# Optimization experiments

Hardware: AMD Instinct MI355X
Metric: run time of the kernel (lower is better)

## Reference

```python
import jax, jax.numpy as jnp
import numpy as np

N_VOCAB_TOTAL = 32064  # n_vocab + n_nts
D_MODEL = 256


def setup_inputs() -> dict:
    key = jax.random.key(0)
    ks = jax.random.split(key, 8)
    d = D_MODEL
    tokens = jax.random.randint(ks[0], (64, 4095), 0, N_VOCAB_TOTAL, dtype=jnp.int32)
    # embedding_tgt: normal with std 1/sqrt(d) (reset_parameters)
    E = jax.random.normal(ks[1], (N_VOCAB_TOTAL, d), dtype=jnp.float32) / jnp.sqrt(jnp.float32(d))
    s_in = 1.0 / np.sqrt(3 * d)
    s_h = 1.0 / np.sqrt(d)
    W_in = jax.random.uniform(ks[2], (d, 3 * d), jnp.float32, -s_in, s_in)  # Linear(3d, d)
    b_in = jax.random.uniform(ks[3], (d,), jnp.float32, -s_in, s_in)
    W1 = jax.random.uniform(ks[4], (d, d), jnp.float32, -s_h, s_h)
    b1 = jax.random.uniform(ks[5], (d,), jnp.float32, -s_h, s_h)
    W2 = jax.random.uniform(ks[6], (d, d), jnp.float32, -s_h, s_h)
    b2 = jax.random.uniform(ks[7], (d,), jnp.float32, -s_h, s_h)
    return {"tokens": tokens, "E": E, "W_in": W_in, "b_in": b_in,
            "W1": W1, "b1": b1, "W2": W2, "b2": b2}


def _bin_agg(roots, left, right, W_in, b_in, W1, b1, W2, b2):
    # skipmlp_binary_agg: root + hidden(inp(cat([root,left,right])))
    # hidden = ELU -> Linear -> ELU -> Linear  (nlayers=2)
    x = jnp.concatenate([roots, left, right], axis=-1)        # [..., 3d]
    h = x @ W_in.T + b_in                                     # inp: Linear(3d, d)
    h = jax.nn.elu(h) @ W1.T + b1
    h = jax.nn.elu(h) @ W2.T + b2
    return roots + h


def reference(tokens, E, W_in, b_in, W1, b1, W2, b2):
    # tokens: [B, N] heap-ordered perfect binary trees, N = 2^(D+1)-1.
    B, N = tokens.shape
    n_leaves = (N + 1) // 2
    emb = E[tokens]                                           # [B, N, d] gather
    cur = emb[:, N - n_leaves:]                               # leaf level, [B, 2^D, d]
    level = n_leaves // 2
    while level >= 1:                                          # fixed D iterations
        roots = emb[:, level - 1: 2 * level - 1]               # [B, level, d]
        left = cur[:, 0::2]
        right = cur[:, 1::2]
        cur = _bin_agg(roots, left, right, W_in, b_in, W1, b1, W2, b2)
        level //= 2
    return cur[:, 0]                                           # [B, d] root embeddings
```

## Files before the change

kernel.cpp:

```cpp
#include <hip/hip_runtime.h>
#include <stdint.h>


typedef __attribute__((ext_vector_type(8))) short short8;
typedef __attribute__((ext_vector_type(4))) float f32x4;

typedef const __attribute__((address_space(1))) unsigned int* gas_ptr;
typedef __attribute__((address_space(3))) unsigned int* las_ptr;

#define TOK_N 4095

__device__ __forceinline__ unsigned short f32_to_bf16(float f) {
    union { float f; unsigned u; } v; v.f = f;
    return (unsigned short)((v.u + 0x7fffu + ((v.u >> 16) & 1u)) >> 16);
}
__device__ __forceinline__ float bf16_to_f32(unsigned short u) {
    union { unsigned u; float f; } v; v.u = ((unsigned)u) << 16; return v.f;
}

__global__ void convert_f32_bf16(const float* __restrict__ E,
                                 const float* __restrict__ Win,
                                 const float* __restrict__ W1,
                                 const float* __restrict__ W2,
                                 unsigned short* __restrict__ Ebf,
                                 unsigned short* __restrict__ Winbf,
                                 unsigned short* __restrict__ W1bf,
                                 unsigned short* __restrict__ W2bf) {
    const int nE = 32064 * 256, nWin = 256 * 768, nW = 256 * 256;
    const int total4 = (nE + nWin + 2 * nW) >> 2;
    for (int i = blockIdx.x * blockDim.x + threadIdx.x; i < total4;
         i += gridDim.x * blockDim.x) {
        int idx = i << 2;
        const float* src; unsigned short* dst; int off;
        if (idx < nE)                  { src = E;   dst = Ebf;   off = idx; }
        else if (idx < nE + nWin)      { src = Win; dst = Winbf; off = idx - nE; }
        else if (idx < nE + nWin + nW) { src = W1;  dst = W1bf;  off = idx - nE - nWin; }
        else                           { src = W2;  dst = W2bf;  off = idx - nE - nWin - nW; }
        float4 f = *(const float4*)(src + off);
        ushort4 o;
        o.x = f32_to_bf16(f.x); o.y = f32_to_bf16(f.y);
        o.z = f32_to_bf16(f.z); o.w = f32_to_bf16(f.w);
        *(ushort4*)(dst + off) = o;
    }
}

template<int MT, int WROW, typename F>
__device__ __forceinline__ void run_pass(const unsigned short* __restrict__ Xs,
                                         const unsigned short* __restrict__ wlane,
                                         int kbase, f32x4 (&acc)[MT][4],
                                         int l15, int q, F&& late)
{
    const int xm = l15 & 7;
    short8 bb[2][4], bt[2][4];
#pragma unroll
    for (int d = 0; d < 2; ++d)
#pragma unroll
        for (int nt = 0; nt < 4; ++nt)
            bb[d][nt] = *(const short8*)(wlane + (size_t)(nt * 16) * WROW + kbase + d * 32);
#pragma unroll
    for (int d = 0; d < 2; ++d)
#pragma unroll
        for (int nt = 0; nt < 4; ++nt)
            bt[d][nt] = *(const short8*)(wlane + (size_t)(nt * 16) * WROW + kbase + (6 + d) * 32);
#pragma unroll
    for (int k = 0; k < 8; ++k) {
        if (k == 4) {
            __builtin_amdgcn_sched_barrier(0);
            late();
            __builtin_amdgcn_sched_barrier(0);
        }
        short8 a[MT];
        const int sl = (((4 * k + q) ^ xm) << 3);
#pragma unroll
        for (int mt = 0; mt < MT; ++mt)
            a[mt] = *(const short8*)(Xs + (mt * 16 + l15) * 256 + sl);
#pragma unroll
        for (int mt = 0; mt < MT; ++mt)
#pragma unroll
            for (int nt = 0; nt < 4; ++nt)
                acc[mt][nt] = __builtin_amdgcn_mfma_f32_16x16x32_bf16(
                    a[mt], (k >= 6) ? bt[k - 6][nt] : bb[k & 1][nt],
                    acc[mt][nt], 0, 0, 0);
        if (k < 4) {
#pragma unroll
            for (int nt = 0; nt < 4; ++nt)
                bb[k & 1][nt] = *(const short8*)(wlane + (size_t)(nt * 16) * WROW + kbase + (k + 2) * 32);
        }
    }
}

template<int MT, int LAST>
__global__ __launch_bounds__(256, 3)
void tree_level(const int* __restrict__ tokens,
                const unsigned short* __restrict__ Ebf,
                const unsigned short* __restrict__ Win,
                const unsigned short* __restrict__ W1,
                const unsigned short* __restrict__ W2,
                const float* __restrict__ b_in,
                const float* __restrict__ b1,
                const float* __restrict__ b2,
                const unsigned short* __restrict__ cur_in,
                unsigned short* __restrict__ cur_out,
                float* __restrict__ final_out,
                int L, int logL, int first)
{
    constexpr int R = MT * 16;
    __shared__ unsigned short Xs[R * 256];
    __shared__ unsigned short Hs[R * 256];
    __shared__ unsigned short Gs[R * 256];

    const int tid  = threadIdx.x;
    const int lane = tid & 63;
    const int wid  = tid >> 6;
    const int l15  = lane & 15;
    const int q    = lane >> 4;
    const int n0   = wid * 64;
    const int blk  = blockIdx.x;

    auto gather = [&](int p, unsigned short* dst) {
#pragma unroll
        for (int t = 0; t < R / 8; ++t) {
            const int base_r = wid * (R / 4) + t * 2;
            const int r = base_r + (lane >> 5);
            const unsigned short* src;
            {
                int g = blk * R + r;
                int b = g >> logL;
                int i = g - (b << logL);
                if (p == 0) {
                    int tok = tokens[b * TOK_N + (L - 1) + i];
                    src = Ebf + (size_t)tok * 256;
                } else if (first) {
                    int tok = tokens[b * TOK_N + 2047 + 2 * i + (p - 1)];
                    src = Ebf + (size_t)tok * 256;
                } else {
                    src = cur_in + ((size_t)b * (2 * L) + 2 * i + (p - 1)) * 256;
                }
            }
            const int c = (lane & 31) ^ (r & 7);
            __builtin_amdgcn_global_load_lds(
                (gas_ptr)(const void*)(src + c * 8),
                (las_ptr)(void*)(dst + base_r * 256), 16, 0, 0);
        }
    };

    float bva[4], bvb[4], bvc[4];
#pragma unroll
    for (int nt = 0; nt < 4; ++nt) {
        bva[nt] = b_in[n0 + nt * 16 + l15];
        bvb[nt] = b1[n0 + nt * 16 + l15];
        bvc[nt] = b2[n0 + nt * 16 + l15];
    }

    f32x4 acc[MT][4];
    auto init_acc = [&](const float* bv) {
#pragma unroll
        for (int mt = 0; mt < MT; ++mt)
#pragma unroll
            for (int nt = 0; nt < 4; ++nt)
                acc[mt][nt] = (f32x4){bv[nt], bv[nt], bv[nt], bv[nt]};
    };
    auto store_elu = [&](unsigned short* dst) {
#pragma unroll
        for (int mt = 0; mt < MT; ++mt)
#pragma unroll
            for (int nt = 0; nt < 4; ++nt)
#pragma unroll
                for (int rr = 0; rr < 4; ++rr) {
                    int row = mt * 16 + q * 4 + rr;
                    int col = n0 + nt * 16 + l15;
                    float h = acc[mt][nt][rr];
                    h = h > 0.f ? h : (__expf(h) - 1.f);
                    int slot = (col >> 3) ^ (row & 7);
                    dst[row * 256 + slot * 8 + (col & 7)] = f32_to_bf16(h);
                }
    };

    gather(0, Xs);
    __syncthreads();
    init_acc(bva);
    const unsigned short* winlane = Win + q * 8 + (size_t)(n0 + l15) * 768;
    run_pass<MT, 768>(Xs, winlane, 0, acc, l15, q, [&]() {
        gather(1, Hs);
        gather(2, Gs);
    });
    __syncthreads();
    run_pass<MT, 768>(Hs, winlane, 256, acc, l15, q, []() {});
    __syncthreads();
    run_pass<MT, 768>(Gs, winlane, 512, acc, l15, q, []() {});
    store_elu(Hs);
    __syncthreads();

    init_acc(bvb);
    run_pass<MT, 256>(Hs, W1 + q * 8 + (size_t)(n0 + l15) * 256, 0, acc, l15, q, []() {});
    __syncthreads();
    store_elu(Hs);
    __syncthreads();

    init_acc(bvc);
    run_pass<MT, 256>(Hs, W2 + q * 8 + (size_t)(n0 + l15) * 256, 0, acc, l15, q, []() {});

    if (LAST) {
#pragma unroll
        for (int mt = 0; mt < MT; ++mt)
#pragma unroll
            for (int nt = 0; nt < 4; ++nt)
#pragma unroll
                for (int rr = 0; rr < 4; ++rr) {
                    int row = mt * 16 + q * 4 + rr;
                    int col = n0 + nt * 16 + l15;
                    int slot = (col >> 3) ^ (row & 7);
                    float o = acc[mt][nt][rr] +
                              bf16_to_f32(Xs[row * 256 + slot * 8 + (col & 7)]);
                    final_out[(size_t)(blk * R + row) * 256 + col] = o;
                }
    } else {
        __syncthreads();
#pragma unroll
        for (int mt = 0; mt < MT; ++mt)
#pragma unroll
            for (int nt = 0; nt < 4; ++nt)
#pragma unroll
                for (int rr = 0; rr < 4; ++rr) {
                    int row = mt * 16 + q * 4 + rr;
                    int col = n0 + nt * 16 + l15;
                    int slot = (col >> 3) ^ (row & 7);
                    float o = acc[mt][nt][rr] +
                              bf16_to_f32(Xs[row * 256 + slot * 8 + (col & 7)]);
                    Gs[row * 256 + slot * 8 + (col & 7)] = f32_to_bf16(o);
                }
        __syncthreads();
        const int s   = tid & 31;
        const int sub = tid >> 5;
#pragma unroll
        for (int it = 0; it < R / 8; ++it) {
            int r = it * 8 + sub;
            int c = s ^ (r & 7);
            *(short8*)(cur_out + (size_t)(blk * R + r) * 256 + c * 8) =
                *(const short8*)(Gs + r * 256 + s * 8);
        }
    }
}

template<int MT, int LAST>
static void launch_level(const int* tokens, const unsigned short* Ebf,
                         const unsigned short* Win, const unsigned short* W1,
                         const unsigned short* W2, const float* b_in,
                         const float* b1, const float* b2,
                         const unsigned short* cin, unsigned short* cout,
                         float* out, int L, int first, hipStream_t stream) {
    int logL = 31 - __builtin_clz((unsigned)L);
    int blocks = (64 * L) / (16 * MT);
    tree_level<MT, LAST><<<dim3(blocks), dim3(256), 0, stream>>>(
        tokens, Ebf, Win, W1, W2, b_in, b1, b2, cin, cout, out, L, logL, first);
}

extern "C" void kernel_launch(void* const* d_in, const int* in_sizes, int n_in,
                              void* d_out, int out_size, void* d_ws, size_t ws_size,
                              hipStream_t stream) {
    const int*   tokens = (const int*)  d_in[0];
    const float* E      = (const float*)d_in[1];
    const float* W_in   = (const float*)d_in[2];
    const float* b_in   = (const float*)d_in[3];
    const float* W1     = (const float*)d_in[4];
    const float* b1     = (const float*)d_in[5];
    const float* W2     = (const float*)d_in[6];
    const float* b2     = (const float*)d_in[7];
    float* out = (float*)d_out;
    char* ws = (char*)d_ws;

    unsigned short* Ebf   = (unsigned short*)(ws);
    unsigned short* Winbf = (unsigned short*)(ws + 16416768);
    unsigned short* W1bf  = (unsigned short*)(ws + 16809984);
    unsigned short* W2bf  = (unsigned short*)(ws + 16941056);
    unsigned short* curA  = (unsigned short*)(ws + 17072128);
    unsigned short* curB  = (unsigned short*)(ws + 50626560);

    convert_f32_bf16<<<1024, 256, 0, stream>>>(E, W_in, W1, W2,
                                               Ebf, Winbf, W1bf, W2bf);

    const unsigned short* cin = curB;
    unsigned short* cout = curA;
    int first = 1;
    for (int L = 1024; L >= 1; L >>= 1) {
        int last = (L == 1);
        if (L >= 256)
            launch_level<2, 0>(tokens, Ebf, Winbf, W1bf, W2bf, b_in, b1, b2,
                               cin, cout, nullptr, L, first, stream);
        else if (!last)
            launch_level<1, 0>(tokens, Ebf, Winbf, W1bf, W2bf, b_in, b1, b2,
                               cin, cout, nullptr, L, first, stream);
        else
            launch_level<1, 1>(tokens, Ebf, Winbf, W1bf, W2bf, b_in, b1, b2,
                               cin, cout, out, L, first, stream);
        cin = cout;
        cout = (cout == curA) ? curB : curA;
        first = 0;
    }
}
```

Measured before the change: 567.0 us.

## Fuse conversion and all tree levels into one persistent cooperative kernel

Replaces the conversion kernel and the eleven per-level launches with a single cooperative persistent kernel that converts weights and embeddings to bf16, then loops over tree levels with grid-wide syncs between them. Blocks stride over 32-row tiles using a rotating three-buffer LDS scheme and prefetch the next tile's root gather during the W1 pass. This removes launch gaps and tail underutilisation on small levels, at the cost of grid.sync overhead and fixed 32-row tiles for the tiny late levels, which leave most blocks idle.

```diff
diff --git a/kernel.cpp b/kernel.cpp
--- a/kernel.cpp
+++ b/kernel.cpp
@@ -1,5 +1,8 @@
 #include <hip/hip_runtime.h>
+#include <hip/hip_cooperative_groups.h>
 #include <stdint.h>
+
+namespace cg = cooperative_groups;
 
 
 typedef __attribute__((ext_vector_type(8))) short short8;
@@ -9,6 +12,7 @@
 typedef __attribute__((address_space(3))) unsigned int* las_ptr;
 
 #define TOK_N 4095
+#define RR 32
 
 __device__ __forceinline__ unsigned short f32_to_bf16(float f) {
     union { float f; unsigned u; } v; v.f = f;
@@ -18,36 +22,10 @@
     union { unsigned u; float f; } v; v.u = ((unsigned)u) << 16; return v.f;
 }
 
-__global__ void convert_f32_bf16(const float* __restrict__ E,
-                                 const float* __restrict__ Win,
-                                 const float* __restrict__ W1,
-                                 const float* __restrict__ W2,
-                                 unsigned short* __restrict__ Ebf,
-                                 unsigned short* __restrict__ Winbf,
-                                 unsigned short* __restrict__ W1bf,
-                                 unsigned short* __restrict__ W2bf) {
-    const int nE = 32064 * 256, nWin = 256 * 768, nW = 256 * 256;
-    const int total4 = (nE + nWin + 2 * nW) >> 2;
-    for (int i = blockIdx.x * blockDim.x + threadIdx.x; i < total4;
-         i += gridDim.x * blockDim.x) {
-        int idx = i << 2;
-        const float* src; unsigned short* dst; int off;
-        if (idx < nE)                  { src = E;   dst = Ebf;   off = idx; }
-        else if (idx < nE + nWin)      { src = Win; dst = Winbf; off = idx - nE; }
-        else if (idx < nE + nWin + nW) { src = W1;  dst = W1bf;  off = idx - nE - nWin; }
-        else                           { src = W2;  dst = W2bf;  off = idx - nE - nWin - nW; }
-        float4 f = *(const float4*)(src + off);
-        ushort4 o;
-        o.x = f32_to_bf16(f.x); o.y = f32_to_bf16(f.y);
-        o.z = f32_to_bf16(f.z); o.w = f32_to_bf16(f.w);
-        *(ushort4*)(dst + off) = o;
-    }
-}
-
-template<int MT, int WROW, typename F>
+template<int WROW, typename F>
 __device__ __forceinline__ void run_pass(const unsigned short* __restrict__ Xs,
                                          const unsigned short* __restrict__ wlane,
-                                         int kbase, f32x4 (&acc)[MT][4],
+                                         int kbase, f32x4 (&acc)[2][4],
                                          int l15, int q, F&& late)
 {
     const int xm = l15 & 7;
@@ -69,13 +47,13 @@
             late();
             __builtin_amdgcn_sched_barrier(0);
         }
-        short8 a[MT];
+        short8 a[2];
         const int sl = (((4 * k + q) ^ xm) << 3);
 #pragma unroll
-        for (int mt = 0; mt < MT; ++mt)
+        for (int mt = 0; mt < 2; ++mt)
             a[mt] = *(const short8*)(Xs + (mt * 16 + l15) * 256 + sl);
 #pragma unroll
-        for (int mt = 0; mt < MT; ++mt)
+        for (int mt = 0; mt < 2; ++mt)
 #pragma unroll
             for (int nt = 0; nt < 4; ++nt)
                 acc[mt][nt] = __builtin_amdgcn_mfma_f32_16x16x32_bf16(
@@ -89,25 +67,46 @@
     }
 }
 
-template<int MT, int LAST>
 __global__ __launch_bounds__(256, 3)
-void tree_level(const int* __restrict__ tokens,
-                const unsigned short* __restrict__ Ebf,
-                const unsigned short* __restrict__ Win,
-                const unsigned short* __restrict__ W1,
-                const unsigned short* __restrict__ W2,
-                const float* __restrict__ b_in,
-                const float* __restrict__ b1,
-                const float* __restrict__ b2,
-                const unsigned short* __restrict__ cur_in,
-                unsigned short* __restrict__ cur_out,
-                float* __restrict__ final_out,
-                int L, int logL, int first)
+void tree_all(const int* __restrict__ tokens,
+              const float* __restrict__ Ef,
+              const float* __restrict__ Winf,
+              const float* __restrict__ b_in,
+              const float* __restrict__ W1f,
+              const float* __restrict__ b1,
+              const float* __restrict__ W2f,
+              const float* __restrict__ b2,
+              unsigned short* __restrict__ Ebf,
+              unsigned short* __restrict__ Win,
+              unsigned short* __restrict__ W1,
+              unsigned short* __restrict__ W2,
+              unsigned short* __restrict__ curA,
+              unsigned short* __restrict__ curB,
+              float* __restrict__ out)
 {
-    constexpr int R = MT * 16;
-    __shared__ unsigned short Xs[R * 256];
-    __shared__ unsigned short Hs[R * 256];
-    __shared__ unsigned short Gs[R * 256];
+    __shared__ unsigned short S[3][RR * 256];
+    cg::grid_group grid = cg::this_grid();
+
+    {
+        const int nE = 32064 * 256, nWin = 256 * 768, nW = 256 * 256;
+        const int total4 = (nE + nWin + 2 * nW) >> 2;
+        for (int i = blockIdx.x * blockDim.x + threadIdx.x; i < total4;
+             i += gridDim.x * blockDim.x) {
+            int idx = i << 2;
+            const float* src; unsigned short* dst; int off;
+            if (idx < nE)                  { src = Ef;  dst = Ebf; off = idx; }
+            else if (idx < nE + nWin)      { src = Winf; dst = Win; off = idx - nE; }
+            else if (idx < nE + nWin + nW) { src = W1f; dst = W1;  off = idx - nE - nWin; }
+            else                           { src = W2f; dst = W2;  off = idx - nE - nWin - nW; }
+            float4 f = *(const float4*)(src + off);
+            ushort4 o;
+            o.x = f32_to_bf16(f.x); o.y = f32_to_bf16(f.y);
+            o.z = f32_to_bf16(f.z); o.w = f32_to_bf16(f.w);
+            *(ushort4*)(dst + off) = o;
+        }
+    }
+    __threadfence();
+    grid.sync();
 
     const int tid  = threadIdx.x;
     const int lane = tid & 63;
@@ -115,34 +114,6 @@
     const int l15  = lane & 15;
     const int q    = lane >> 4;
     const int n0   = wid * 64;
-    const int blk  = blockIdx.x;
-
-    auto gather = [&](int p, unsigned short* dst) {
-#pragma unroll
-        for (int t = 0; t < R / 8; ++t) {
-            const int base_r = wid * (R / 4) + t * 2;
-            const int r = base_r + (lane >> 5);
-            const unsigned short* src;
-            {
-                int g = blk * R + r;
-                int b = g >> logL;
-                int i = g - (b << logL);
-                if (p == 0) {
-                    int tok = tokens[b * TOK_N + (L - 1) + i];
-                    src = Ebf + (size_t)tok * 256;
-                } else if (first) {
-                    int tok = tokens[b * TOK_N + 2047 + 2 * i + (p - 1)];
-                    src = Ebf + (size_t)tok * 256;
-                } else {
-                    src = cur_in + ((size_t)b * (2 * L) + 2 * i + (p - 1)) * 256;
-                }
-            }
-            const int c = (lane & 31) ^ (r & 7);
-            __builtin_amdgcn_global_load_lds(
-                (gas_ptr)(const void*)(src + c * 8),
-                (las_ptr)(void*)(dst + base_r * 256), 16, 0, 0);
-        }
-    };
 
     float bva[4], bvb[4], bvc[4];
 #pragma unroll
@@ -151,18 +122,21 @@
         bvb[nt] = b1[n0 + nt * 16 + l15];
         bvc[nt] = b2[n0 + nt * 16 + l15];
     }
-
-    f32x4 acc[MT][4];
+    const unsigned short* winlane = Win + q * 8 + (size_t)(n0 + l15) * 768;
+    const unsigned short* w1lane  = W1  + q * 8 + (size_t)(n0 + l15) * 256;
+    const unsigned short* w2lane  = W2  + q * 8 + (size_t)(n0 + l15) * 256;
+
+    f32x4 acc[2][4];
     auto init_acc = [&](const float* bv) {
 #pragma unroll
-        for (int mt = 0; mt < MT; ++mt)
+        for (int mt = 0; mt < 2; ++mt)
 #pragma unroll
             for (int nt = 0; nt < 4; ++nt)
                 acc[mt][nt] = (f32x4){bv[nt], bv[nt], bv[nt], bv[nt]};
     };
     auto store_elu = [&](unsigned short* dst) {
 #pragma unroll
-        for (int mt = 0; mt < MT; ++mt)
+        for (int mt = 0; mt < 2; ++mt)
 #pragma unroll
             for (int nt = 0; nt < 4; ++nt)
 #pragma unroll
@@ -176,83 +150,118 @@
                 }
     };
 
-    gather(0, Xs);
-    __syncthreads();
-    init_acc(bva);
-    const unsigned short* winlane = Win + q * 8 + (size_t)(n0 + l15) * 768;
-    run_pass<MT, 768>(Xs, winlane, 0, acc, l15, q, [&]() {
-        gather(1, Hs);
-        gather(2, Gs);
-    });
-    __syncthreads();
-    run_pass<MT, 768>(Hs, winlane, 256, acc, l15, q, []() {});
-    __syncthreads();
-    run_pass<MT, 768>(Gs, winlane, 512, acc, l15, q, []() {});
-    store_elu(Hs);
-    __syncthreads();
-
-    init_acc(bvb);
-    run_pass<MT, 256>(Hs, W1 + q * 8 + (size_t)(n0 + l15) * 256, 0, acc, l15, q, []() {});
-    __syncthreads();
-    store_elu(Hs);
-    __syncthreads();
-
-    init_acc(bvc);
-    run_pass<MT, 256>(Hs, W2 + q * 8 + (size_t)(n0 + l15) * 256, 0, acc, l15, q, []() {});
-
-    if (LAST) {
-#pragma unroll
-        for (int mt = 0; mt < MT; ++mt)
-#pragma unroll
-            for (int nt = 0; nt < 4; ++nt)
-#pragma unroll
-                for (int rr = 0; rr < 4; ++rr) {
-                    int row = mt * 16 + q * 4 + rr;
-                    int col = n0 + nt * 16 + l15;
-                    int slot = (col >> 3) ^ (row & 7);
-                    float o = acc[mt][nt][rr] +
-                              bf16_to_f32(Xs[row * 256 + slot * 8 + (col & 7)]);
-                    final_out[(size_t)(blk * R + row) * 256 + col] = o;
+    int r = 0, l = 1, m = 2;
+    const unsigned short* cin = curB;
+    unsigned short* cout = curA;
+
+    for (int L = 1024; L >= 1; L >>= 1) {
+        const int logL  = 31 - __builtin_clz((unsigned)L);
+        const int tiles = 2 * L;
+        const int first = (L == 1024);
+        const int last  = (L == 1);
+
+        auto gather = [&](int p, int tile, unsigned short* dst) {
+#pragma unroll
+            for (int it = 0; it < RR / 8; ++it) {
+                const int base_r = wid * (RR / 4) + it * 2;
+                const int rw = base_r + (lane >> 5);
+                const unsigned short* src;
+                {
+                    int g = tile * RR + rw;
+                    int b = g >> logL;
+                    int i = g - (b << logL);
+                    if (p == 0) {
+                        int tok = tokens[b * TOK_N + (L - 1) + i];
+                        src = Ebf + (size_t)tok * 256;
+                    } else if (first) {
+                        int tok = tokens[b * TOK_N + 2047 + 2 * i + (p - 1)];
+                        src = Ebf + (size_t)tok * 256;
+                    } else {
+                        src = cin + ((size_t)b * (2 * L) + 2 * i + (p - 1)) * 256;
+                    }
                 }
-    } else {
-        __syncthreads();
-#pragma unroll
-        for (int mt = 0; mt < MT; ++mt)
-#pragma unroll
-            for (int nt = 0; nt < 4; ++nt)
-#pragma unroll
-                for (int rr = 0; rr < 4; ++rr) {
-                    int row = mt * 16 + q * 4 + rr;
-                    int col = n0 + nt * 16 + l15;
-                    int slot = (col >> 3) ^ (row & 7);
-                    float o = acc[mt][nt][rr] +
-                              bf16_to_f32(Xs[row * 256 + slot * 8 + (col & 7)]);
-                    Gs[row * 256 + slot * 8 + (col & 7)] = f32_to_bf16(o);
+                const int c = (lane & 31) ^ (rw & 7);
+                __builtin_amdgcn_global_load_lds(
+                    (gas_ptr)(const void*)(src + c * 8),
+                    (las_ptr)(void*)(dst + base_r * 256), 16, 0, 0);
+            }
+        };
+
+        int t = blockIdx.x;
+        if (t < tiles) gather(0, t, S[r]);
+        for (; t < tiles; t += gridDim.x) {
+            __syncthreads();
+
+            init_acc(bva);
+            run_pass<768>(S[r], winlane, 0, acc, l15, q, [&]() {
+                gather(1, t, S[l]);
+                gather(2, t, S[m]);
+            });
+            __syncthreads();
+            run_pass<768>(S[l], winlane, 256, acc, l15, q, []() {});
+            __syncthreads();
+            run_pass<768>(S[m], winlane, 512, acc, l15, q, []() {});
+            store_elu(S[l]);
+            __syncthreads();
+
+            init_acc(bvb);
+            const bool pre = (t + (int)gridDim.x) < tiles;
+            run_pass<256>(S[l], w1lane, 0, acc, l15, q, [&]() {
+                if (pre) gather(0, t + gridDim.x, S[m]);
+            });
+            __syncthreads();
+            store_elu(S[l]);
+            __syncthreads();
+
+            init_acc(bvc);
+            run_pass<256>(S[l], w2lane, 0, acc, l15, q, []() {});
+
+            if (last) {
+#pragma unroll
+                for (int mt = 0; mt < 2; ++mt)
+#pragma unroll
+                    for (int nt = 0; nt < 4; ++nt)
+#pragma unroll
+                        for (int rr = 0; rr < 4; ++rr) {
+                            int row = mt * 16 + q * 4 + rr;
+                            int col = n0 + nt * 16 + l15;
+                            int slot = (col >> 3) ^ (row & 7);
+                            float o = acc[mt][nt][rr] +
+                                      bf16_to_f32(S[r][row * 256 + slot * 8 + (col & 7)]);
+                            out[(size_t)(t * RR + row) * 256 + col] = o;
+                        }
+            } else {
+#pragma unroll
+                for (int mt = 0; mt < 2; ++mt)
+#pragma unroll
+                    for (int nt = 0; nt < 4; ++nt)
+#pragma unroll
+                        for (int rr = 0; rr < 4; ++rr) {
+                            int row = mt * 16 + q * 4 + rr;
+                            int col = n0 + nt * 16 + l15;
+                            int slot = (col >> 3) ^ (row & 7);
+                            int a = row * 256 + slot * 8 + (col & 7);
+                            float o = acc[mt][nt][rr] + bf16_to_f32(S[r][a]);
+                            S[r][a] = f32_to_bf16(o);
+                        }
+                __syncthreads();
+                const int s   = tid & 31;
+                const int sub = tid >> 5;
+#pragma unroll
+                for (int it = 0; it < RR / 8; ++it) {
+                    int rw = it * 8 + sub;
+                    int c = s ^ (rw & 7);
+                    *(short8*)(cout + (size_t)(t * RR + rw) * 256 + c * 8) =
+                        *(const short8*)(S[r] + rw * 256 + s * 8);
                 }
-        __syncthreads();
-        const int s   = tid & 31;
-        const int sub = tid >> 5;
-#pragma unroll
-        for (int it = 0; it < R / 8; ++it) {
-            int r = it * 8 + sub;
-            int c = s ^ (r & 7);
-            *(short8*)(cur_out + (size_t)(blk * R + r) * 256 + c * 8) =
-                *(const short8*)(Gs + r * 256 + s * 8);
+            }
+            int nr = m; m = l; l = r; r = nr;
         }
+        __threadfence();
+        grid.sync();
+        cin = cout;
+        cout = (cout == curA) ? curB : curA;
     }
-}
-
-template<int MT, int LAST>
-static void launch_level(const int* tokens, const unsigned short* Ebf,
-                         const unsigned short* Win, const unsigned short* W1,
-                         const unsigned short* W2, const float* b_in,
-                         const float* b1, const float* b2,
-                         const unsigned short* cin, unsigned short* cout,
-                         float* out, int L, int first, hipStream_t stream) {
-    int logL = 31 - __builtin_clz((unsigned)L);
-    int blocks = (64 * L) / (16 * MT);
-    tree_level<MT, LAST><<<dim3(blocks), dim3(256), 0, stream>>>(
-        tokens, Ebf, Win, W1, W2, b_in, b1, b2, cin, cout, out, L, logL, first);
 }
 
 extern "C" void kernel_launch(void* const* d_in, const int* in_sizes, int n_in,
@@ -276,25 +285,16 @@
     unsigned short* curA  = (unsigned short*)(ws + 17072128);
     unsigned short* curB  = (unsigned short*)(ws + 50626560);
 
-    convert_f32_bf16<<<1024, 256, 0, stream>>>(E, W_in, W1, W2,
-                                               Ebf, Winbf, W1bf, W2bf);
-
-    const unsigned short* cin = curB;
-    unsigned short* cout = curA;
-    int first = 1;
-    for (int L = 1024; L >= 1; L >>= 1) {
-        int last = (L == 1);
-        if (L >= 256)
-            launch_level<2, 0>(tokens, Ebf, Winbf, W1bf, W2bf, b_in, b1, b2,
-                               cin, cout, nullptr, L, first, stream);
-        else if (!last)
-            launch_level<1, 0>(tokens, Ebf, Winbf, W1bf, W2bf, b_in, b1, b2,
-                               cin, cout, nullptr, L, first, stream);
-        else
-            launch_level<1, 1>(tokens, Ebf, Winbf, W1bf, W2bf, b_in, b1, b2,
-                               cin, cout, out, L, first, stream);
-        cin = cout;
-        cout = (cout == curA) ? curB : curA;
-        first = 0;
-    }
-}
+    int maxB = 0;
+    hipOccupancyMaxActiveBlocksPerMultiprocessor(&maxB, (const void*)tree_all, 256, 0);
+    if (maxB < 1) maxB = 1;
+    if (maxB > 3) maxB = 3;
+    int grid = 256 * maxB;
+
+    void* args[] = { (void*)&tokens, (void*)&E, (void*)&W_in, (void*)&b_in,
+                     (void*)&W1, (void*)&b1, (void*)&W2, (void*)&b2,
+                     (void*)&Ebf, (void*)&Winbf, (void*)&W1bf, (void*)&W2bf,
+                     (void*)&curA, (void*)&curB, (void*)&out };
+    hipLaunchCooperativeKernel((const void*)tree_all, dim3(grid), dim3(256),
+                               args, 0, stream);
+}
```

Result: slower. 1.905 ms (+235.9%).

## Fuse small tree levels into one per-batch tail kernel and prefetch weights across passes

Applied to the files above, without the earlier changes.

Levels 32 and below now run in a single tree_tail kernel, one block per batch element. Intermediate results stay in shared memory across levels, which removes six kernel launches and their global round trips. The weight-fragment pipeline is rewritten as a 4-deep register ring that preloads the next matrix's first K-slices during the current pass, so the next GEMM does not stall on weight loads. All tree_level launches are fixed at 32 rows per block. The tail kernel has only 64 blocks and computes padded rows for small levels, so it runs at low occupancy and does wasted work.

```diff
diff --git a/kernel.cpp b/kernel.cpp
--- a/kernel.cpp
+++ b/kernel.cpp
@@ -9,6 +9,7 @@
 typedef __attribute__((address_space(3))) unsigned int* las_ptr;
 
 #define TOK_N 4095
+#define RR 32
 
 __device__ __forceinline__ unsigned short f32_to_bf16(float f) {
     union { float f; unsigned u; } v; v.f = f;
@@ -44,24 +45,16 @@
     }
 }
 
-template<int MT, int WROW, typename F>
+template<typename F>
 __device__ __forceinline__ void run_pass(const unsigned short* __restrict__ Xs,
-                                         const unsigned short* __restrict__ wlane,
-                                         int kbase, f32x4 (&acc)[MT][4],
+                                         const unsigned short* __restrict__ curW,
+                                         int curNT, int curK,
+                                         const unsigned short* __restrict__ nxtW,
+                                         int nxtNT, int nxtK, bool hasNext,
+                                         short8 (&bb)[4][4], f32x4 (&acc)[2][4],
                                          int l15, int q, F&& late)
 {
     const int xm = l15 & 7;
-    short8 bb[2][4], bt[2][4];
-#pragma unroll
-    for (int d = 0; d < 2; ++d)
-#pragma unroll
-        for (int nt = 0; nt < 4; ++nt)
-            bb[d][nt] = *(const short8*)(wlane + (size_t)(nt * 16) * WROW + kbase + d * 32);
-#pragma unroll
-    for (int d = 0; d < 2; ++d)
-#pragma unroll
-        for (int nt = 0; nt < 4; ++nt)
-            bt[d][nt] = *(const short8*)(wlane + (size_t)(nt * 16) * WROW + kbase + (6 + d) * 32);
 #pragma unroll
     for (int k = 0; k < 8; ++k) {
         if (k == 4) {
@@ -69,27 +62,31 @@
             late();
             __builtin_amdgcn_sched_barrier(0);
         }
-        short8 a[MT];
+        short8 a0, a1;
         const int sl = (((4 * k + q) ^ xm) << 3);
-#pragma unroll
-        for (int mt = 0; mt < MT; ++mt)
-            a[mt] = *(const short8*)(Xs + (mt * 16 + l15) * 256 + sl);
-#pragma unroll
-        for (int mt = 0; mt < MT; ++mt)
-#pragma unroll
-            for (int nt = 0; nt < 4; ++nt)
-                acc[mt][nt] = __builtin_amdgcn_mfma_f32_16x16x32_bf16(
-                    a[mt], (k >= 6) ? bt[k - 6][nt] : bb[k & 1][nt],
-                    acc[mt][nt], 0, 0, 0);
+        a0 = *(const short8*)(Xs + l15 * 256 + sl);
+        a1 = *(const short8*)(Xs + (16 + l15) * 256 + sl);
+        short8 bc[4];
+#pragma unroll
+        for (int nt = 0; nt < 4; ++nt) bc[nt] = bb[k & 3][nt];
+#pragma unroll
+        for (int nt = 0; nt < 4; ++nt)
+            acc[0][nt] = __builtin_amdgcn_mfma_f32_16x16x32_bf16(a0, bc[nt], acc[0][nt], 0, 0, 0);
+#pragma unroll
+        for (int nt = 0; nt < 4; ++nt)
+            acc[1][nt] = __builtin_amdgcn_mfma_f32_16x16x32_bf16(a1, bc[nt], acc[1][nt], 0, 0, 0);
         if (k < 4) {
 #pragma unroll
             for (int nt = 0; nt < 4; ++nt)
-                bb[k & 1][nt] = *(const short8*)(wlane + (size_t)(nt * 16) * WROW + kbase + (k + 2) * 32);
-        }
-    }
-}
-
-template<int MT, int LAST>
+                bb[k & 3][nt] = *(const short8*)(curW + nt * curNT + curK + (k + 4) * 32);
+        } else if (hasNext) {
+#pragma unroll
+            for (int nt = 0; nt < 4; ++nt)
+                bb[k & 3][nt] = *(const short8*)(nxtW + nt * nxtNT + nxtK + (k - 4) * 32);
+        }
+    }
+}
+
 __global__ __launch_bounds__(256, 3)
 void tree_level(const int* __restrict__ tokens,
                 const unsigned short* __restrict__ Ebf,
@@ -101,13 +98,11 @@
                 const float* __restrict__ b2,
                 const unsigned short* __restrict__ cur_in,
                 unsigned short* __restrict__ cur_out,
-                float* __restrict__ final_out,
                 int L, int logL, int first)
 {
-    constexpr int R = MT * 16;
-    __shared__ unsigned short Xs[R * 256];
-    __shared__ unsigned short Hs[R * 256];
-    __shared__ unsigned short Gs[R * 256];
+    __shared__ unsigned short S0[RR * 256];
+    __shared__ unsigned short S1[RR * 256];
+    __shared__ unsigned short S2[RR * 256];
 
     const int tid  = threadIdx.x;
     const int lane = tid & 63;
@@ -116,15 +111,17 @@
     const int q    = lane >> 4;
     const int n0   = wid * 64;
     const int blk  = blockIdx.x;
+    const int s    = tid & 31;
+    const int sub  = tid >> 5;
 
     auto gather = [&](int p, unsigned short* dst) {
 #pragma unroll
-        for (int t = 0; t < R / 8; ++t) {
-            const int base_r = wid * (R / 4) + t * 2;
+        for (int it = 0; it < 4; ++it) {
+            const int base_r = wid * 8 + it * 2;
             const int r = base_r + (lane >> 5);
             const unsigned short* src;
             {
-                int g = blk * R + r;
+                int g = blk * RR + r;
                 int b = g >> logL;
                 int i = g - (b << logL);
                 if (p == 0) {
@@ -151,18 +148,21 @@
         bvb[nt] = b1[n0 + nt * 16 + l15];
         bvc[nt] = b2[n0 + nt * 16 + l15];
     }
-
-    f32x4 acc[MT][4];
+    const unsigned short* winlane = Win + q * 8 + (size_t)(n0 + l15) * 768;
+    const unsigned short* w1lane  = W1  + q * 8 + (size_t)(n0 + l15) * 256;
+    const unsigned short* w2lane  = W2  + q * 8 + (size_t)(n0 + l15) * 256;
+
+    f32x4 acc[2][4];
     auto init_acc = [&](const float* bv) {
 #pragma unroll
-        for (int mt = 0; mt < MT; ++mt)
+        for (int mt = 0; mt < 2; ++mt)
 #pragma unroll
             for (int nt = 0; nt < 4; ++nt)
                 acc[mt][nt] = (f32x4){bv[nt], bv[nt], bv[nt], bv[nt]};
     };
     auto store_elu = [&](unsigned short* dst) {
 #pragma unroll
-        for (int mt = 0; mt < MT; ++mt)
+        for (int mt = 0; mt < 2; ++mt)
 #pragma unroll
             for (int nt = 0; nt < 4; ++nt)
 #pragma unroll
@@ -176,83 +176,232 @@
                 }
     };
 
-    gather(0, Xs);
-    __syncthreads();
+    short8 bb[4][4];
+    auto noop = []() {};
+
+    gather(0, S0);
+#pragma unroll
+    for (int j = 0; j < 4; ++j)
+#pragma unroll
+        for (int nt = 0; nt < 4; ++nt)
+            bb[j][nt] = *(const short8*)(winlane + nt * 12288 + j * 32);
+    __syncthreads();
+
     init_acc(bva);
+    run_pass(S0, winlane, 12288, 0, winlane, 12288, 256, true, bb, acc, l15, q,
+             [&]() { gather(1, S1); gather(2, S2); });
+    __syncthreads();
+    run_pass(S1, winlane, 12288, 256, winlane, 12288, 512, true, bb, acc, l15, q, noop);
+    run_pass(S2, winlane, 12288, 512, w1lane, 4096, 0, true, bb, acc, l15, q, noop);
+    __syncthreads();
+    store_elu(S1);
+    __syncthreads();
+
+    init_acc(bvb);
+    run_pass(S1, w1lane, 4096, 0, w2lane, 4096, 0, true, bb, acc, l15, q, noop);
+    __syncthreads();
+    store_elu(S1);
+    __syncthreads();
+
+    init_acc(bvc);
+    run_pass(S1, w2lane, 4096, 0, (const unsigned short*)nullptr, 0, 0, false,
+             bb, acc, l15, q, noop);
+
+#pragma unroll
+    for (int mt = 0; mt < 2; ++mt)
+#pragma unroll
+        for (int nt = 0; nt < 4; ++nt)
+#pragma unroll
+            for (int rr = 0; rr < 4; ++rr) {
+                int row = mt * 16 + q * 4 + rr;
+                int col = n0 + nt * 16 + l15;
+                int slot = (col >> 3) ^ (row & 7);
+                float o = acc[mt][nt][rr] +
+                          bf16_to_f32(S0[row * 256 + slot * 8 + (col & 7)]);
+                S1[row * 256 + slot * 8 + (col & 7)] = f32_to_bf16(o);
+            }
+    __syncthreads();
+#pragma unroll
+    for (int it = 0; it < 4; ++it) {
+        int r = it * 8 + sub;
+        int c = s ^ (r & 7);
+        *(short8*)(cur_out + (size_t)(blk * RR + r) * 256 + c * 8) =
+            *(const short8*)(S1 + r * 256 + s * 8);
+    }
+}
+
+__global__ __launch_bounds__(256, 2)
+void tree_tail(const int* __restrict__ tokens,
+               const unsigned short* __restrict__ Ebf,
+               const unsigned short* __restrict__ Win,
+               const unsigned short* __restrict__ W1,
+               const unsigned short* __restrict__ W2,
+               const float* __restrict__ b_in,
+               const float* __restrict__ b1,
+               const float* __restrict__ b2,
+               const unsigned short* __restrict__ cur_in,
+               float* __restrict__ out)
+{
+    __shared__ unsigned short S0[RR * 256];
+    __shared__ unsigned short S1[RR * 256];
+    __shared__ unsigned short S2[RR * 256];
+    __shared__ unsigned short P[RR * 256];
+
+    const int b    = blockIdx.x;
+    const int tid  = threadIdx.x;
+    const int lane = tid & 63;
+    const int wid  = tid >> 6;
+    const int l15  = lane & 15;
+    const int q    = lane >> 4;
+    const int n0   = wid * 64;
+    const int s    = tid & 31;
+    const int sub  = tid >> 5;
+
+    float bva[4], bvb[4], bvc[4];
+#pragma unroll
+    for (int nt = 0; nt < 4; ++nt) {
+        bva[nt] = b_in[n0 + nt * 16 + l15];
+        bvb[nt] = b1[n0 + nt * 16 + l15];
+        bvc[nt] = b2[n0 + nt * 16 + l15];
+    }
     const unsigned short* winlane = Win + q * 8 + (size_t)(n0 + l15) * 768;
-    run_pass<MT, 768>(Xs, winlane, 0, acc, l15, q, [&]() {
-        gather(1, Hs);
-        gather(2, Gs);
-    });
-    __syncthreads();
-    run_pass<MT, 768>(Hs, winlane, 256, acc, l15, q, []() {});
-    __syncthreads();
-    run_pass<MT, 768>(Gs, winlane, 512, acc, l15, q, []() {});
-    store_elu(Hs);
-    __syncthreads();
-
-    init_acc(bvb);
-    run_pass<MT, 256>(Hs, W1 + q * 8 + (size_t)(n0 + l15) * 256, 0, acc, l15, q, []() {});
-    __syncthreads();
-    store_elu(Hs);
-    __syncthreads();
-
-    init_acc(bvc);
-    run_pass<MT, 256>(Hs, W2 + q * 8 + (size_t)(n0 + l15) * 256, 0, acc, l15, q, []() {});
-
-    if (LAST) {
-#pragma unroll
-        for (int mt = 0; mt < MT; ++mt)
+    const unsigned short* w1lane  = W1  + q * 8 + (size_t)(n0 + l15) * 256;
+    const unsigned short* w2lane  = W2  + q * 8 + (size_t)(n0 + l15) * 256;
+
+    f32x4 acc[2][4];
+    auto init_acc = [&](const float* bv) {
+#pragma unroll
+        for (int mt = 0; mt < 2; ++mt)
+#pragma unroll
+            for (int nt = 0; nt < 4; ++nt)
+                acc[mt][nt] = (f32x4){bv[nt], bv[nt], bv[nt], bv[nt]};
+    };
+    auto store_elu = [&](unsigned short* dst) {
+#pragma unroll
+        for (int mt = 0; mt < 2; ++mt)
 #pragma unroll
             for (int nt = 0; nt < 4; ++nt)
 #pragma unroll
                 for (int rr = 0; rr < 4; ++rr) {
                     int row = mt * 16 + q * 4 + rr;
                     int col = n0 + nt * 16 + l15;
+                    float h = acc[mt][nt][rr];
+                    h = h > 0.f ? h : (__expf(h) - 1.f);
                     int slot = (col >> 3) ^ (row & 7);
-                    float o = acc[mt][nt][rr] +
-                              bf16_to_f32(Xs[row * 256 + slot * 8 + (col & 7)]);
-                    final_out[(size_t)(blk * R + row) * 256 + col] = o;
+                    dst[row * 256 + slot * 8 + (col & 7)] = f32_to_bf16(h);
                 }
-    } else {
+    };
+
+    short8 bb[4][4];
+    auto noop = []() {};
+
+    auto groot = [&](int L) {
+#pragma unroll
+        for (int it = 0; it < 4; ++it) {
+            const int base_r = wid * 8 + it * 2;
+            const int r = base_r + (lane >> 5);
+            const int i = (r < L) ? r : 0;
+            int tok = tokens[b * TOK_N + (L - 1) + i];
+            const unsigned short* src = Ebf + (size_t)tok * 256;
+            const int c = (lane & 31) ^ (r & 7);
+            __builtin_amdgcn_global_load_lds(
+                (gas_ptr)(const void*)(src + c * 8),
+                (las_ptr)(void*)(S0 + base_r * 256), 16, 0, 0);
+        }
+    };
+    auto gchild_g = [&](int p, unsigned short* dst) {
+#pragma unroll
+        for (int it = 0; it < 4; ++it) {
+            const int base_r = wid * 8 + it * 2;
+            const int r = base_r + (lane >> 5);
+            const unsigned short* src = cur_in + ((size_t)b * 64 + 2 * r + (p - 1)) * 256;
+            const int c = (lane & 31) ^ (r & 7);
+            __builtin_amdgcn_global_load_lds(
+                (gas_ptr)(const void*)(src + c * 8),
+                (las_ptr)(void*)(dst + base_r * 256), 16, 0, 0);
+        }
+    };
+    auto gchild_p = [&](int L) {
+#pragma unroll
+        for (int it = 0; it < 4; ++it) {
+            int r = it * 8 + sub;
+            int i = (r < L) ? r : 0;
+            int c = s ^ (r & 7);
+            int sl = 2 * i, sr = 2 * i + 1;
+            *(short8*)(S1 + r * 256 + s * 8) = *(const short8*)(P + sl * 256 + ((c ^ (sl & 7))) * 8);
+            *(short8*)(S2 + r * 256 + s * 8) = *(const short8*)(P + sr * 256 + ((c ^ (sr & 7))) * 8);
+        }
+    };
+
+#pragma unroll
+    for (int j = 0; j < 4; ++j)
+#pragma unroll
+        for (int nt = 0; nt < 4; ++nt)
+            bb[j][nt] = *(const short8*)(winlane + nt * 12288 + j * 32);
+
+    for (int L = 32; L >= 1; L >>= 1) {
+        const bool lastJob = (L == 1);
+        groot(L);
+        if (L == 32) { gchild_g(1, S1); gchild_g(2, S2); }
+        else         gchild_p(L);
         __syncthreads();
-#pragma unroll
-        for (int mt = 0; mt < MT; ++mt)
-#pragma unroll
-            for (int nt = 0; nt < 4; ++nt)
-#pragma unroll
-                for (int rr = 0; rr < 4; ++rr) {
-                    int row = mt * 16 + q * 4 + rr;
-                    int col = n0 + nt * 16 + l15;
-                    int slot = (col >> 3) ^ (row & 7);
-                    float o = acc[mt][nt][rr] +
-                              bf16_to_f32(Xs[row * 256 + slot * 8 + (col & 7)]);
-                    Gs[row * 256 + slot * 8 + (col & 7)] = f32_to_bf16(o);
-                }
+
+        init_acc(bva);
+        run_pass(S0, winlane, 12288, 0, winlane, 12288, 256, true, bb, acc, l15, q, noop);
+        run_pass(S1, winlane, 12288, 256, winlane, 12288, 512, true, bb, acc, l15, q, noop);
+        run_pass(S2, winlane, 12288, 512, w1lane, 4096, 0, true, bb, acc, l15, q, noop);
         __syncthreads();
-        const int s   = tid & 31;
-        const int sub = tid >> 5;
-#pragma unroll
-        for (int it = 0; it < R / 8; ++it) {
-            int r = it * 8 + sub;
-            int c = s ^ (r & 7);
-            *(short8*)(cur_out + (size_t)(blk * R + r) * 256 + c * 8) =
-                *(const short8*)(Gs + r * 256 + s * 8);
-        }
-    }
-}
-
-template<int MT, int LAST>
-static void launch_level(const int* tokens, const unsigned short* Ebf,
-                         const unsigned short* Win, const unsigned short* W1,
-                         const unsigned short* W2, const float* b_in,
-                         const float* b1, const float* b2,
-                         const unsigned short* cin, unsigned short* cout,
-                         float* out, int L, int first, hipStream_t stream) {
-    int logL = 31 - __builtin_clz((unsigned)L);
-    int blocks = (64 * L) / (16 * MT);
-    tree_level<MT, LAST><<<dim3(blocks), dim3(256), 0, stream>>>(
-        tokens, Ebf, Win, W1, W2, b_in, b1, b2, cin, cout, out, L, logL, first);
+        store_elu(S1);
+        __syncthreads();
+
+        init_acc(bvb);
+        run_pass(S1, w1lane, 4096, 0, w2lane, 4096, 0, true, bb, acc, l15, q, noop);
+        __syncthreads();
+        store_elu(S1);
+        __syncthreads();
+
+        init_acc(bvc);
+        run_pass(S1, w2lane, 4096, 0, winlane, 12288, 0, !lastJob, bb, acc, l15, q, noop);
+
+        if (lastJob) {
+#pragma unroll
+            for (int mt = 0; mt < 2; ++mt)
+#pragma unroll
+                for (int nt = 0; nt < 4; ++nt)
+#pragma unroll
+                    for (int rr = 0; rr < 4; ++rr) {
+                        int row = mt * 16 + q * 4 + rr;
+                        if (row != 0) continue;
+                        int col = n0 + nt * 16 + l15;
+                        int slot = (col >> 3) ^ (row & 7);
+                        float o = acc[mt][nt][rr] +
+                                  bf16_to_f32(S0[row * 256 + slot * 8 + (col & 7)]);
+                        out[(size_t)b * 256 + col] = o;
+                    }
+        } else {
+#pragma unroll
+            for (int mt = 0; mt < 2; ++mt)
+#pragma unroll
+                for (int nt = 0; nt < 4; ++nt)
+#pragma unroll
+                    for (int rr = 0; rr < 4; ++rr) {
+                        int row = mt * 16 + q * 4 + rr;
+                        int col = n0 + nt * 16 + l15;
+                        int slot = (col >> 3) ^ (row & 7);
+                        float o = acc[mt][nt][rr] +
+                                  bf16_to_f32(S0[row * 256 + slot * 8 + (col & 7)]);
+                        S1[row * 256 + slot * 8 + (col & 7)] = f32_to_bf16(o);
+                    }
+            __syncthreads();
+#pragma unroll
+            for (int it = 0; it < 4; ++it) {
+                int r = it * 8 + sub;
+                if (r < L)
+                    *(short8*)(P + r * 256 + s * 8) = *(const short8*)(S1 + r * 256 + s * 8);
+            }
+            __syncthreads();
+        }
+    }
 }
 
 extern "C" void kernel_launch(void* const* d_in, const int* in_sizes, int n_in,
@@ -282,19 +431,14 @@
     const unsigned short* cin = curB;
     unsigned short* cout = curA;
     int first = 1;
-    for (int L = 1024; L >= 1; L >>= 1) {
-        int last = (L == 1);
-        if (L >= 256)
-            launch_level<2, 0>(tokens, Ebf, Winbf, W1bf, W2bf, b_in, b1, b2,
-                               cin, cout, nullptr, L, first, stream);
-        else if (!last)
-            launch_level<1, 0>(tokens, Ebf, Winbf, W1bf, W2bf, b_in, b1, b2,
-                               cin, cout, nullptr, L, first, stream);
-        else
-            launch_level<1, 1>(tokens, Ebf, Winbf, W1bf, W2bf, b_in, b1, b2,
-                               cin, cout, out, L, first, stream);
+    for (int L = 1024; L >= 64; L >>= 1) {
+        int logL = 31 - __builtin_clz((unsigned)L);
+        tree_level<<<dim3(2 * L), dim3(256), 0, stream>>>(
+            tokens, Ebf, Winbf, W1bf, W2bf, b_in, b1, b2, cin, cout, L, logL, first);
         cin = cout;
         cout = (cout == curA) ? curB : curA;
         first = 0;
     }
-}
+    tree_tail<<<dim3(64), dim3(256), 0, stream>>>(
+        tokens, Ebf, Winbf, W1bf, W2bf, b_in, b1, b2, cin, out);
+}
```

Result: slower. 745.4 us (+31.5%).
